# Optimization experiments

Hardware: AMD Instinct MI355X
Metric: run time of the kernel (lower is better)

Reference implementation:

```python
import jax, jax.numpy as jnp
import numpy as np

A2B = 1.8897259886          # angstrom -> bohr
EV2HA = 0.0367493
NUM_RBF = 16
R_MIN = 0.5 * A2B
R_MAX = 4.0 * A2B           # r_max_angstroms=4.0 from gnn_config
RBF_WIDTH = (R_MAX - R_MIN) / NUM_RBF
N_NODES = 100_000
N_EDGES = 3_200_000
EMBED_DIM = 16
N_ELEMS = 4
CODES_PER_ELEM = 4          # all elements are core -> max_codes_per_element
TOTAL_CODES = N_ELEMS * CODES_PER_ELEM
NUM_PAIRS = 10
CODE_OWNER = np.repeat(np.arange(N_ELEMS), CODES_PER_ELEM)  # element owning each code


def setup_inputs() -> dict:
    key = jax.random.key(0)
    ks = jax.random.split(key, 12)
    N, E, D = N_NODES, N_EDGES, EMBED_DIM
    inv_sp = lambda v: np.float32(np.log(np.expm1(v)))  # inverse_softplus
    return {
        "elem_idx": jax.random.randint(ks[0], (N,), 0, N_ELEMS),
        "edge_index": jax.random.randint(ks[1], (2, E), 0, N),
        "distances": jax.random.uniform(ks[2], (E,), minval=1.0, maxval=7.5),  # bohr
        "pair_idx": jax.random.randint(ks[3], (E,), 0, NUM_PAIRS),
        "embed": jax.random.normal(ks[4], (N_ELEMS, D)),
        "fw1": jax.random.normal(ks[5], (D, NUM_RBF)) * 0.3,
        "fb1": jnp.zeros((D,)),
        "fw2": jax.random.normal(ks[6], (D, D)) * 0.3,
        "fb2": jnp.zeros((D,)),
        "mw1": jax.random.normal(ks[7], (D, D)) * 0.3,
        "mb1": jnp.zeros((D,)),
        "mw2": jax.random.normal(ks[8], (3, D)) * 0.05,  # zero-init in orig; small random for a live baseline
        "mb2": jnp.zeros((3,)),
        "codebook": jax.random.normal(ks[9], (TOTAL_CODES, D)),
        "raw_D_e": jnp.full((NUM_PAIRS,), inv_sp(0.1 * EV2HA)),
        "raw_alpha": jnp.full((NUM_PAIRS,), inv_sp(1.5 / A2B)),
        "raw_r0": jnp.full((NUM_PAIRS,), np.float32(3.0 * A2B)),
    }


def reference(elem_idx, edge_index, distances, pair_idx, embed,
              fw1, fb1, fw2, fb2, mw1, mb1, mw2, mb2,
              codebook, raw_D_e, raw_alpha, raw_r0):
    # --- EnvironmentEncoder: gather + edge filter + scatter_add ---
    h = embed[elem_idx]                                              # [N, D]
    centers = jnp.linspace(R_MIN, R_MAX, NUM_RBF, dtype=distances.dtype)
    rbf = jnp.exp(-0.5 * ((distances[:, None] - centers) / RBF_WIDTH) ** 2)  # [E, RBF]
    W = jax.nn.silu(rbf @ fw1.T + fb1) @ fw2.T + fb2                 # [E, D]
    src, tgt = edge_index[0], edge_index[1]
    messages = h[tgt] * W                                            # [E, D]
    agg = jax.ops.segment_sum(messages, src, num_segments=h.shape[0])
    h = h + agg                                                      # [N, D]

    # --- VectorQuantizer (eval path): per-element masked cdist + argmin ---
    d2 = (jnp.sum(h * h, axis=1, keepdims=True)
          - 2.0 * h @ codebook.T
          + jnp.sum(codebook * codebook, axis=1))                    # [N, C] squared dist
    owner = jnp.asarray(CODE_OWNER)
    valid = elem_idx[:, None] == owner[None, :]                      # [N, C]
    atom_types = jnp.argmin(jnp.where(valid, d2, jnp.inf), axis=1)   # [N]
    z_q = codebook[atom_types]                                       # [N, D]
    h_q = h + jax.lax.stop_gradient(z_q - h)                         # straight-through
    # all elements have >1 code -> commitment over all atoms
    vq_loss = 0.25 * jnp.mean((h - jax.lax.stop_gradient(z_q)) ** 2)

    # --- MorseParameterPredictor: edge gather + MLP ---
    pair_feat = h_q[src] + h_q[tgt]                                  # [E, D]
    delta = jax.nn.silu(pair_feat @ mw1.T + mb1) @ mw2.T + mb2       # [E, 3]

    D_e = jax.nn.softplus(raw_D_e[pair_idx] + delta[:, 0])
    alpha = jax.nn.softplus(raw_alpha[pair_idx] + delta[:, 1])
    r0 = raw_r0[pair_idx] + delta[:, 2]
    params = jnp.stack([D_e, alpha, r0], axis=-1)                    # [E, 3]
    return params, vq_loss
```

## Files before the change

kernel.cpp:

```cpp
#include <hip/hip_runtime.h>
#include <stdint.h>

#define A2B   1.8897259886f
#define R_MIN (0.5f * A2B)
#define R_MAX (4.0f * A2B)

#define EPB 2048

__global__ void __launch_bounds__(256) k_bucket(
        const int* __restrict__ src, const int* __restrict__ tgt,
        const int* __restrict__ elem, const float* __restrict__ dist,
        int* __restrict__ gCursor, float* __restrict__ dBuf,
        unsigned short* __restrict__ kBuf, int CAP, int SHIFT, int E)
{
    __shared__ int cnt[256], base_[256];
    int t = threadIdx.x;
    cnt[t] = 0;
    __syncthreads();
    int e0 = blockIdx.x * EPB;
    int eEnd = (e0 + EPB < E) ? e0 + EPB : E;

    float dv[8]; int bv[8]; unsigned short kv[8];
    #pragma unroll
    for (int j = 0; j < 8; ++j) {
        int e = e0 + t + j * 256;
        if (e < eEnd) {
            int s = src[e];
            int q = elem[tgt[e]];
            dv[j] = dist[e];
            int b = s >> SHIFT;
            bv[j] = b;
            kv[j] = (unsigned short)(((s - (b << SHIFT)) << 2) | q);
            atomicAdd(&cnt[b], 1);
        }
    }
    __syncthreads();
    if (cnt[t] > 0) base_[t] = atomicAdd(&gCursor[t], cnt[t]);
    __syncthreads();
    cnt[t] = 0;
    __syncthreads();
    #pragma unroll
    for (int j = 0; j < 8; ++j) {
        int e = e0 + t + j * 256;
        if (e < eEnd) {
            int b = bv[j];
            int pos = base_[b] + atomicAdd(&cnt[b], 1);
            if (pos < CAP) {
                size_t idx = (size_t)b * CAP + pos;
                dBuf[idx] = dv[j];
                kBuf[idx] = kv[j];
            }
        }
    }
}

__global__ void __launch_bounds__(256) k_bscan(
        const int* __restrict__ gCursor, int* __restrict__ bucketBase,
        int* __restrict__ offs, int NBUK, int N, int E)
{
    __shared__ int sd[256];
    int t = threadIdx.x;
    int v = (t < NBUK) ? gCursor[t] : 0;
    sd[t] = v; __syncthreads();
    #pragma unroll
    for (int o = 1; o < 256; o <<= 1) {
        int x = (t >= o) ? sd[t - o] : 0;
        __syncthreads();
        sd[t] += x;
        __syncthreads();
    }
    bucketBase[t] = sd[t] - v;
    if (t == 0) offs[N] = E;
}

__global__ void __launch_bounds__(256) k_bin(
        const float* __restrict__ dBuf, const unsigned short* __restrict__ kBuf,
        const int* __restrict__ gCursor, const int* __restrict__ bucketBase,
        int* __restrict__ offs, float* __restrict__ payload,
        int CAP, int SHIFT, int N)
{
    __shared__ int lcnt[512];
    __shared__ int sd[256];
    int t = threadIdx.x, b = blockIdx.x;
    int n0 = b << SHIFT;
    int n1 = n0 + (1 << SHIFT); if (n1 > N) n1 = N;
    int m  = n1 - n0;
    int cntE = gCursor[b]; if (cntE > CAP) cntE = CAP;
    int base = bucketBase[b];
    for (int i = t; i < m; i += 256) lcnt[i] = 0;
    __syncthreads();
    const float* dB = dBuf + (size_t)b * CAP;
    const unsigned short* kB = kBuf + (size_t)b * CAP;
    for (int i = t; i < cntE; i += 256)
        atomicAdd(&lcnt[kB[i] >> 2], 1);
    __syncthreads();
    int b2 = t * 2;
    int v0 = (b2 < m)     ? lcnt[b2]     : 0;
    int v1 = (b2 + 1 < m) ? lcnt[b2 + 1] : 0;
    int tsum = v0 + v1;
    sd[t] = tsum; __syncthreads();
    #pragma unroll
    for (int o = 1; o < 256; o <<= 1) {
        int x = (t >= o) ? sd[t - o] : 0;
        __syncthreads();
        sd[t] += x;
        __syncthreads();
    }
    int run = sd[t] - tsum;
    if (b2 < m)     { lcnt[b2] = run;     offs[n0 + b2] = base + run;     run += v0; }
    if (b2 + 1 < m) { lcnt[b2 + 1] = run; offs[n0 + b2 + 1] = base + run; run += v1; }
    __syncthreads();
    for (int i = t; i < cntE; i += 256) {
        int kv = kB[i];
        int pos = atomicAdd(&lcnt[kv >> 2], 1);
        unsigned db = __float_as_uint(dB[i]);
        payload[base + pos] = __uint_as_float((db & ~3u) | (unsigned)(kv & 3));
    }
}

__global__ void __launch_bounds__(256) k_gather(
        const int* __restrict__ elem, const float* __restrict__ embed,
        const float* __restrict__ codebook,
        const float* __restrict__ fw1, const float* __restrict__ fb1,
        const float* __restrict__ fw2, const float* __restrict__ fb2,
        const int* __restrict__ offs, const float* __restrict__ payload,
        int* __restrict__ atype, float* __restrict__ loss, int N)
{
    __shared__ float4 s_fw1t[64];
    __shared__ float4 s_fw2v[64];
    __shared__ float s_cb[256];
    __shared__ float s_fb1[16], s_fb2[16], s_emb[64], s_cbn[16];
    __shared__ float s_red[4];
    int t = threadIdx.x;
    {
        float* f1 = (float*)s_fw1t;
        f1[(t & 15) * 16 + (t >> 4)] = fw1[t];
        float* f2 = (float*)s_fw2v;
        f2[t] = fw2[t];
        s_cb[t] = codebook[t];
    }
    if (t < 16) { s_fb1[t] = fb1[t]; s_fb2[t] = fb2[t]; }
    if (t < 64) s_emb[t] = embed[t];
    __syncthreads();
    if (t < 16) {
        float s = 0.f;
        #pragma unroll
        for (int j = 0; j < 16; ++j) { float c = s_cb[t * 16 + j]; s += c * c; }
        s_cbn[t] = s;
    }
    __syncthreads();

    int node = blockIdx.x * 64 + (t >> 2);
    int sub  = t & 3;
    float lp = 0.0f;
    if (node < N) {
        int o0 = offs[node], o1 = offs[node + 1];
        float G0[16], G1[16], G2[16], G3[16];
        #pragma unroll
        for (int j = 0; j < 16; ++j) { G0[j]=0.f; G1[j]=0.f; G2[j]=0.f; G3[j]=0.f; }
        float c0 = 0.f, c1 = 0.f, c2 = 0.f, c3 = 0.f;

        const float invw   = 16.0f / (R_MAX - R_MIN);
        const float u0base = R_MIN * invw;
        const float kstep  = 16.0f / 15.0f;
        for (int i = o0 + sub; i < o1; i += 8) {
            int ii = i + 4;
            bool has2 = (ii < o1);
            unsigned p0 = __float_as_uint(payload[i]);
            unsigned p1 = has2 ? __float_as_uint(payload[ii]) : p0;
            int q0 = (int)(p0 & 3u), q1 = (int)(p1 & 3u);
            float d0 = __uint_as_float(p0 & ~3u);
            float d1 = __uint_as_float(p1 & ~3u);
            float ua = d0 * invw - u0base;
            float ub = d1 * invw - u0base;
            float g0[16], g1[16];
            #pragma unroll
            for (int i2 = 0; i2 < 16; ++i2) { g0[i2] = s_fb1[i2]; g1[i2] = s_fb1[i2]; }
            #pragma clang loop unroll(disable)
            for (int k = 0; k < 16; ++k) {
                float r0 = __expf(-0.5f * ua * ua);
                float r1 = __expf(-0.5f * ub * ub);
                float4 w0 = s_fw1t[k*4+0], w1 = s_fw1t[k*4+1];
                float4 w2 = s_fw1t[k*4+2], w3 = s_fw1t[k*4+3];
                g0[0]+=r0*w0.x;  g0[1]+=r0*w0.y;  g0[2]+=r0*w0.z;  g0[3]+=r0*w0.w;
                g0[4]+=r0*w1.x;  g0[5]+=r0*w1.y;  g0[6]+=r0*w1.z;  g0[7]+=r0*w1.w;
                g0[8]+=r0*w2.x;  g0[9]+=r0*w2.y;  g0[10]+=r0*w2.z; g0[11]+=r0*w2.w;
                g0[12]+=r0*w3.x; g0[13]+=r0*w3.y; g0[14]+=r0*w3.z; g0[15]+=r0*w3.w;
                g1[0]+=r1*w0.x;  g1[1]+=r1*w0.y;  g1[2]+=r1*w0.z;  g1[3]+=r1*w0.w;
                g1[4]+=r1*w1.x;  g1[5]+=r1*w1.y;  g1[6]+=r1*w1.z;  g1[7]+=r1*w1.w;
                g1[8]+=r1*w2.x;  g1[9]+=r1*w2.y;  g1[10]+=r1*w2.z; g1[11]+=r1*w2.w;
                g1[12]+=r1*w3.x; g1[13]+=r1*w3.y; g1[14]+=r1*w3.z; g1[15]+=r1*w3.w;
                ua -= kstep; ub -= kstep;
            }
            {
                float m0 = (q0==0)?1.f:0.f, m1 = (q0==1)?1.f:0.f;
                float m2 = (q0==2)?1.f:0.f, m3 = (q0==3)?1.f:0.f;
                c0 += m0; c1 += m1; c2 += m2; c3 += m3;
                #pragma unroll
                for (int i2 = 0; i2 < 16; ++i2) {
                    float a = g0[i2];
                    float s = a * __builtin_amdgcn_rcpf(1.0f + __expf(-a));
                    G0[i2] += m0*s; G1[i2] += m1*s; G2[i2] += m2*s; G3[i2] += m3*s;
                }
            }
            if (has2) {
                float m0 = (q1==0)?1.f:0.f, m1 = (q1==1)?1.f:0.f;
                float m2 = (q1==2)?1.f:0.f, m3 = (q1==3)?1.f:0.f;
                c0 += m0; c1 += m1; c2 += m2; c3 += m3;
                #pragma unroll
                for (int i2 = 0; i2 < 16; ++i2) {
                    float a = g1[i2];
                    float s = a * __builtin_amdgcn_rcpf(1.0f + __expf(-a));
                    G0[i2] += m0*s; G1[i2] += m1*s; G2[i2] += m2*s; G3[i2] += m3*s;
                }
            }
        }
        #pragma unroll
        for (int mm = 1; mm <= 2; mm <<= 1) {
            #pragma unroll
            for (int j = 0; j < 16; ++j) {
                G0[j] += __shfl_xor(G0[j], mm, 64);
                G1[j] += __shfl_xor(G1[j], mm, 64);
                G2[j] += __shfl_xor(G2[j], mm, 64);
                G3[j] += __shfl_xor(G3[j], mm, 64);
            }
            c0 += __shfl_xor(c0, mm, 64);
            c1 += __shfl_xor(c1, mm, 64);
            c2 += __shfl_xor(c2, mm, 64);
            c3 += __shfl_xor(c3, mm, 64);
        }
        float Gs[16];
        #pragma unroll
        for (int j = 0; j < 16; ++j)
            Gs[j] = (sub==0) ? G0[j] : (sub==1) ? G1[j] : (sub==2) ? G2[j] : G3[j];
        float cs = (sub==0) ? c0 : (sub==1) ? c1 : (sub==2) ? c2 : c3;
        const float* er = s_emb + sub * 16;
        float acc[16];
        #pragma clang loop unroll_count(4)
        for (int j = 0; j < 16; ++j) {
            float4 f0 = s_fw2v[j*4+0], f1 = s_fw2v[j*4+1];
            float4 f2 = s_fw2v[j*4+2], f3 = s_fw2v[j*4+3];
            float w = Gs[0]*f0.x  + Gs[1]*f0.y  + Gs[2]*f0.z  + Gs[3]*f0.w
                    + Gs[4]*f1.x  + Gs[5]*f1.y  + Gs[6]*f1.z  + Gs[7]*f1.w
                    + Gs[8]*f2.x  + Gs[9]*f2.y  + Gs[10]*f2.z + Gs[11]*f2.w
                    + Gs[12]*f3.x + Gs[13]*f3.y + Gs[14]*f3.z + Gs[15]*f3.w;
            acc[j] = (w + cs * s_fb2[j]) * er[j];
        }
        #pragma unroll
        for (int mm = 1; mm <= 2; mm <<= 1) {
            #pragma unroll
            for (int j = 0; j < 16; ++j)
                acc[j] += __shfl_xor(acc[j], mm, 64);
        }
        int qn = elem[node];
        float h[16], hh = 0.f;
        #pragma unroll
        for (int j = 0; j < 16; ++j) {
            h[j] = acc[j] + s_emb[qn * 16 + j];
            hh += h[j] * h[j];
        }
        float best = __builtin_inff(); int bi = 0;
        #pragma unroll
        for (int c = 0; c < 4; ++c) {
            int code = qn * 4 + c;
            float dot = 0.f;
            #pragma unroll
            for (int j = 0; j < 16; ++j) dot += h[j] * s_cb[code * 16 + j];
            float d2 = hh - 2.0f * dot + s_cbn[code];
            if (d2 < best) { best = d2; bi = code; }
        }
        if (sub == 0) {
            atype[node] = bi;
            #pragma unroll
            for (int j = 0; j < 16; ++j) {
                float df = h[j] - s_cb[bi * 16 + j];
                lp += df * df;
            }
        }
    }
    #pragma unroll
    for (int o = 32; o > 0; o >>= 1) lp += __shfl_down(lp, o, 64);
    int wid = t >> 6;
    if ((t & 63) == 0) s_red[wid] = lp;
    __syncthreads();
    if (t == 0) atomicAdd(loss, s_red[0] + s_red[1] + s_red[2] + s_red[3]);
}

__global__ void __launch_bounds__(256) k_table(
        const float* __restrict__ codebook,
        const float* __restrict__ mw1, const float* __restrict__ mb1,
        const float* __restrict__ mw2, const float* __restrict__ mb2,
        const float* __restrict__ rD, const float* __restrict__ rA,
        const float* __restrict__ rR,
        const float* __restrict__ loss, float4* __restrict__ table,
        float* __restrict__ out_loss, float inv_nd)
{
    __shared__ float s_cb[256], s_mw1[256], s_mb1[16], s_mw2[48], s_mb2[3];
    __shared__ float s_rd[10], s_ra[10], s_rr[10];
    int tid = threadIdx.x;
    s_cb[tid] = codebook[tid];
    s_mw1[tid] = mw1[tid];
    if (tid < 16) s_mb1[tid] = mb1[tid];
    if (tid < 48) s_mw2[tid] = mw2[tid];
    if (tid < 3)  s_mb2[tid] = mb2[tid];
    if (tid < 10) { s_rd[tid] = rD[tid]; s_ra[tid] = rA[tid]; s_rr[tid] = rR[tid]; }
    __syncthreads();

    int a = tid >> 4, b = tid & 15;
    float pf[16];
    #pragma unroll
    for (int j = 0; j < 16; ++j) pf[j] = s_cb[a * 16 + j] + s_cb[b * 16 + j];
    float hid[16];
    #pragma unroll
    for (int i = 0; i < 16; ++i) {
        float acc = s_mb1[i];
        #pragma unroll
        for (int j = 0; j < 16; ++j) acc += pf[j] * s_mw1[i * 16 + j];
        hid[i] = acc / (1.0f + __expf(-acc));
    }
    float del[3];
    #pragma unroll
    for (int r = 0; r < 3; ++r) {
        float acc = s_mb2[r];
        #pragma unroll
        for (int i = 0; i < 16; ++i) acc += hid[i] * s_mw2[r * 16 + i];
        del[r] = acc;
    }
    #pragma unroll
    for (int p = 0; p < 10; ++p) {
        float xd = s_rd[p] + del[0];
        float xa = s_ra[p] + del[1];
        float De = (xd > 20.f) ? xd : log1pf(__expf(xd));
        float al = (xa > 20.f) ? xa : log1pf(__expf(xa));
        float r0 = s_rr[p] + del[2];
        table[tid * 10 + p] = make_float4(De, al, r0, 0.f);
    }
    if (tid == 0) out_loss[0] = 0.25f * loss[0] * inv_nd;
}

__global__ void __launch_bounds__(256) k_out(
        const int* __restrict__ src, const int* __restrict__ tgt,
        const int* __restrict__ pidx, const int* __restrict__ atype,
        const float4* __restrict__ table, float2* __restrict__ out, int Ehalf)
{
    int i = blockIdx.x * 256 + threadIdx.x;
    if (i >= Ehalf) return;
    int2 s2 = ((const int2*)src)[i];
    int2 t2 = ((const int2*)tgt)[i];
    int2 p2 = ((const int2*)pidx)[i];
    int i0 = (atype[s2.x] * 16 + atype[t2.x]) * 10 + p2.x;
    int i1 = (atype[s2.y] * 16 + atype[t2.y]) * 10 + p2.y;
    float4 t0 = table[i0];
    float4 t1 = table[i1];
    float2* op = out + (size_t)3 * i;
    op[0] = make_float2(t0.x, t0.y);
    op[1] = make_float2(t0.z, t1.x);
    op[2] = make_float2(t1.y, t1.z);
}

extern "C" void kernel_launch(void* const* d_in, const int* in_sizes, int n_in,
                              void* d_out, int out_size, void* d_ws, size_t ws_size,
                              hipStream_t stream)
{
    (void)n_in;
    const int*   elem  = (const int*)d_in[0];
    const int*   eidx  = (const int*)d_in[1];
    const float* dist  = (const float*)d_in[2];
    const int*   pidx  = (const int*)d_in[3];
    const float* embed = (const float*)d_in[4];
    const float* fw1   = (const float*)d_in[5];
    const float* fb1   = (const float*)d_in[6];
    const float* fw2   = (const float*)d_in[7];
    const float* fb2   = (const float*)d_in[8];
    const float* mw1   = (const float*)d_in[9];
    const float* mb1   = (const float*)d_in[10];
    const float* mw2   = (const float*)d_in[11];
    const float* mb2   = (const float*)d_in[12];
    const float* cb    = (const float*)d_in[13];
    const float* rD    = (const float*)d_in[14];
    const float* rA    = (const float*)d_in[15];
    const float* rR    = (const float*)d_in[16];

    int N = in_sizes[0];
    int E = in_sizes[2];
    const int* src = eidx;
    const int* tgt = eidx + E;

    int SHIFT = 0;
    while ((1 << SHIFT) < (N + 255) / 256) SHIFT++;
    int NBUK = (N + (1 << SHIFT) - 1) >> SHIFT;
    long long expv = ((long long)E << SHIFT) / N;
    int CAP = (int)(expv + expv / 16 + 256);

    size_t outBytes = (size_t)out_size * 4;
    char* ob = (char*)d_out;
    size_t oc = 0;
    float* dBuf = (float*)(ob + oc);           oc += (size_t)NBUK * CAP * 4;
    unsigned short* kBuf = (unsigned short*)(ob + oc); oc += (size_t)NBUK * CAP * 2;
    oc = (oc + 3) & ~(size_t)3;
    float* payload = (float*)(ob + oc);        oc += (size_t)E * 4;
    int*   offs    = (int*)(ob + oc);          oc += (size_t)(N + 1) * 4;
    if (oc > outBytes) return;

    char* ws = (char*)d_ws;
    size_t cur = 0;
    int*   gCursor    = (int*)(ws + cur);  cur += 256 * 4;
    float* loss       = (float*)(ws + cur); cur += 4;
    size_t clearB = cur;
    int*   bucketBase = (int*)(ws + cur);  cur += 256 * 4;
    int*   atype      = (int*)(ws + cur);  cur += (size_t)N * 4;
    cur = (cur + 15) & ~(size_t)15;
    float4* table     = (float4*)(ws + cur); cur += 2560 * sizeof(float4);
    if (ws_size < cur) return;

    hipMemsetAsync(d_ws, 0, clearB, stream);

    k_bucket<<<(E + EPB - 1) / EPB, 256, 0, stream>>>(
        src, tgt, elem, dist, gCursor, dBuf, kBuf, CAP, SHIFT, E);
    k_bscan<<<1, 256, 0, stream>>>(gCursor, bucketBase, offs, NBUK, N, E);
    k_bin<<<NBUK, 256, 0, stream>>>(dBuf, kBuf, gCursor, bucketBase,
                                    offs, payload, CAP, SHIFT, N);
    k_gather<<<(N + 63) / 64, 256, 0, stream>>>(elem, embed, cb, fw1, fb1,
                                                fw2, fb2, offs, payload,
                                                atype, loss, N);
    float* outl = (float*)d_out + (size_t)3 * E;
    k_table<<<1, 256, 0, stream>>>(cb, mw1, mb1, mw2, mb2, rD, rA, rR,
                                   loss, table, outl,
                                   1.0f / (float)((size_t)N * 16));
    k_out<<<(E / 2 + 255) / 256, 256, 0, stream>>>(src, tgt, pidx, atype, table,
                                                   (float2*)d_out, E / 2);
}
```

Baseline: 259.7 us.

## Privatize per-wave bucket counters and degree-sort nodes within gather blocks

The bucketing kernel now keeps a separate shared counter array for each wavefront, which cuts LDS atomic contention, and derives per-wave base offsets from a single global atomic per bucket. The gather kernel bitonic-sorts its 64 nodes by degree in shared memory and assigns them to wavefronts in that order, so nodes with similar edge counts share a wave and lanes sit idle less often. The cost is extra shared memory and about 21 barrier-separated sort steps per block.

```diff
diff --git a/kernel.cpp b/kernel.cpp
--- a/kernel.cpp
+++ b/kernel.cpp
@@ -13,9 +13,10 @@
         int* __restrict__ gCursor, float* __restrict__ dBuf,
         unsigned short* __restrict__ kBuf, int CAP, int SHIFT, int E)
 {
-    __shared__ int cnt[256], base_[256];
+    __shared__ int cnt[4][256], sbase[4][256];
     int t = threadIdx.x;
-    cnt[t] = 0;
+    int w = t >> 6;
+    cnt[0][t] = 0; cnt[1][t] = 0; cnt[2][t] = 0; cnt[3][t] = 0;
     __syncthreads();
     int e0 = blockIdx.x * EPB;
     int eEnd = (e0 + EPB < E) ? e0 + EPB : E;
@@ -31,20 +32,27 @@
             int b = s >> SHIFT;
             bv[j] = b;
             kv[j] = (unsigned short)(((s - (b << SHIFT)) << 2) | q);
-            atomicAdd(&cnt[b], 1);
-        }
-    }
-    __syncthreads();
-    if (cnt[t] > 0) base_[t] = atomicAdd(&gCursor[t], cnt[t]);
-    __syncthreads();
-    cnt[t] = 0;
+            atomicAdd(&cnt[w][b], 1);
+        }
+    }
+    __syncthreads();
+    {
+        int c0 = cnt[0][t], c1 = cnt[1][t], c2 = cnt[2][t], c3 = cnt[3][t];
+        int tot = c0 + c1 + c2 + c3;
+        int g = (tot > 0) ? atomicAdd(&gCursor[t], tot) : 0;
+        sbase[0][t] = g;
+        sbase[1][t] = g + c0;
+        sbase[2][t] = g + c0 + c1;
+        sbase[3][t] = g + c0 + c1 + c2;
+        cnt[0][t] = 0; cnt[1][t] = 0; cnt[2][t] = 0; cnt[3][t] = 0;
+    }
     __syncthreads();
     #pragma unroll
     for (int j = 0; j < 8; ++j) {
         int e = e0 + t + j * 256;
         if (e < eEnd) {
             int b = bv[j];
-            int pos = base_[b] + atomicAdd(&cnt[b], 1);
+            int pos = sbase[w][b] + atomicAdd(&cnt[w][b], 1);
             if (pos < CAP) {
                 size_t idx = (size_t)b * CAP + pos;
                 dBuf[idx] = dv[j];
@@ -131,6 +139,7 @@
     __shared__ float s_cb[256];
     __shared__ float s_fb1[16], s_fb2[16], s_emb[64], s_cbn[16];
     __shared__ float s_red[4];
+    __shared__ int s_ord[64];
     int t = threadIdx.x;
     {
         float* f1 = (float*)s_fw1t;
@@ -141,6 +150,12 @@
     }
     if (t < 16) { s_fb1[t] = fb1[t]; s_fb2[t] = fb2[t]; }
     if (t < 64) s_emb[t] = embed[t];
+    int nbase = blockIdx.x * 64;
+    if (t < 64) {
+        int n = nbase + t;
+        int dg = (n < N) ? (offs[n + 1] - offs[n]) : 0x7FFF;
+        s_ord[t] = (dg << 6) | t;
+    }
     __syncthreads();
     if (t < 16) {
         float s = 0.f;
@@ -148,9 +163,22 @@
         for (int j = 0; j < 16; ++j) { float c = s_cb[t * 16 + j]; s += c * c; }
         s_cbn[t] = s;
     }
-    __syncthreads();
-
-    int node = blockIdx.x * 64 + (t >> 2);
+    for (int ksz = 2; ksz <= 64; ksz <<= 1) {
+        for (int jj = ksz >> 1; jj > 0; jj >>= 1) {
+            __syncthreads();
+            if (t < 64) {
+                int ixj = t ^ jj;
+                if (ixj > t) {
+                    int a = s_ord[t], b = s_ord[ixj];
+                    bool asc = ((t & ksz) == 0);
+                    if (asc ? (a > b) : (a < b)) { s_ord[t] = b; s_ord[ixj] = a; }
+                }
+            }
+        }
+    }
+    __syncthreads();
+
+    int node = nbase + (s_ord[t >> 2] & 63);
     int sub  = t & 3;
     float lp = 0.0f;
     if (node < N) {
```

Measured after the change: 255.5 us. No clear change (-1.6%).

## Fuse binning into gather with 128-node buckets sorted in shared memory

Applied to the files above, without the earlier changes.

Replaces the three-pass bucket/scan/bin pipeline with a single coarse bucketing pass into 128-node buckets, then has each gather block do the local histogram, prefix scan and scatter of payloads into shared memory before computing. Nodes within a block are bitonic-sorted by degree so the four lanes per node see balanced work. This removes two kernel launches and the global payload/offs round trip. In exchange, k_bucket reads src twice, the fw1 filter weights are read from global memory instead of LDS, the per-bucket capacity is clamped to the shared buffer size so overflow edges would be dropped, and the large shared buffer may limit occupancy.

```diff
diff --git a/kernel.cpp b/kernel.cpp
--- a/kernel.cpp
+++ b/kernel.cpp
@@ -5,142 +5,71 @@
 #define R_MIN (0.5f * A2B)
 #define R_MAX (4.0f * A2B)
 
-#define EPB 2048
+#define EPB   16384
+#define BSH   7
+#define BN    128
 
 __global__ void __launch_bounds__(256) k_bucket(
         const int* __restrict__ src, const int* __restrict__ tgt,
         const int* __restrict__ elem, const float* __restrict__ dist,
+        const float* __restrict__ fw1, float* __restrict__ fw1t,
         int* __restrict__ gCursor, float* __restrict__ dBuf,
-        unsigned short* __restrict__ kBuf, int CAP, int SHIFT, int E)
+        unsigned char* __restrict__ lBuf, int CAP, int NBUK, int E)
 {
-    __shared__ int cnt[256], base_[256];
+    __shared__ int cnt[1024], sbase[1024];
     int t = threadIdx.x;
-    cnt[t] = 0;
+    if (blockIdx.x == 0)
+        fw1t[t] = fw1[(t & 15) * 16 + (t >> 4)];
+    for (int i = t; i < NBUK; i += 256) cnt[i] = 0;
     __syncthreads();
     int e0 = blockIdx.x * EPB;
     int eEnd = (e0 + EPB < E) ? e0 + EPB : E;
-
-    float dv[8]; int bv[8]; unsigned short kv[8];
-    #pragma unroll
-    for (int j = 0; j < 8; ++j) {
-        int e = e0 + t + j * 256;
-        if (e < eEnd) {
-            int s = src[e];
-            int q = elem[tgt[e]];
-            dv[j] = dist[e];
-            int b = s >> SHIFT;
-            bv[j] = b;
-            kv[j] = (unsigned short)(((s - (b << SHIFT)) << 2) | q);
-            atomicAdd(&cnt[b], 1);
-        }
-    }
-    __syncthreads();
-    if (cnt[t] > 0) base_[t] = atomicAdd(&gCursor[t], cnt[t]);
-    __syncthreads();
-    cnt[t] = 0;
-    __syncthreads();
-    #pragma unroll
-    for (int j = 0; j < 8; ++j) {
-        int e = e0 + t + j * 256;
-        if (e < eEnd) {
-            int b = bv[j];
-            int pos = base_[b] + atomicAdd(&cnt[b], 1);
-            if (pos < CAP) {
-                size_t idx = (size_t)b * CAP + pos;
-                dBuf[idx] = dv[j];
-                kBuf[idx] = kv[j];
-            }
+    for (int e = e0 + t; e < eEnd; e += 256)
+        atomicAdd(&cnt[src[e] >> BSH], 1);
+    __syncthreads();
+    for (int i = t; i < NBUK; i += 256) {
+        int c = cnt[i];
+        sbase[i] = c ? atomicAdd(&gCursor[i], c) : 0;
+        cnt[i] = 0;
+    }
+    __syncthreads();
+    for (int e = e0 + t; e < eEnd; e += 256) {
+        int s = src[e];
+        int b = s >> BSH;
+        int q = elem[tgt[e]];
+        float d = dist[e];
+        int pos = sbase[b] + atomicAdd(&cnt[b], 1);
+        if (pos < CAP) {
+            size_t idx = (size_t)b * CAP + pos;
+            dBuf[idx] = __uint_as_float((__float_as_uint(d) & ~3u) | (unsigned)q);
+            lBuf[idx] = (unsigned char)(s & (BN - 1));
         }
     }
 }
 
-__global__ void __launch_bounds__(256) k_bscan(
-        const int* __restrict__ gCursor, int* __restrict__ bucketBase,
-        int* __restrict__ offs, int NBUK, int N, int E)
-{
-    __shared__ int sd[256];
-    int t = threadIdx.x;
-    int v = (t < NBUK) ? gCursor[t] : 0;
-    sd[t] = v; __syncthreads();
-    #pragma unroll
-    for (int o = 1; o < 256; o <<= 1) {
-        int x = (t >= o) ? sd[t - o] : 0;
-        __syncthreads();
-        sd[t] += x;
-        __syncthreads();
-    }
-    bucketBase[t] = sd[t] - v;
-    if (t == 0) offs[N] = E;
-}
-
-__global__ void __launch_bounds__(256) k_bin(
-        const float* __restrict__ dBuf, const unsigned short* __restrict__ kBuf,
-        const int* __restrict__ gCursor, const int* __restrict__ bucketBase,
-        int* __restrict__ offs, float* __restrict__ payload,
-        int CAP, int SHIFT, int N)
-{
-    __shared__ int lcnt[512];
-    __shared__ int sd[256];
-    int t = threadIdx.x, b = blockIdx.x;
-    int n0 = b << SHIFT;
-    int n1 = n0 + (1 << SHIFT); if (n1 > N) n1 = N;
-    int m  = n1 - n0;
-    int cntE = gCursor[b]; if (cntE > CAP) cntE = CAP;
-    int base = bucketBase[b];
-    for (int i = t; i < m; i += 256) lcnt[i] = 0;
-    __syncthreads();
-    const float* dB = dBuf + (size_t)b * CAP;
-    const unsigned short* kB = kBuf + (size_t)b * CAP;
-    for (int i = t; i < cntE; i += 256)
-        atomicAdd(&lcnt[kB[i] >> 2], 1);
-    __syncthreads();
-    int b2 = t * 2;
-    int v0 = (b2 < m)     ? lcnt[b2]     : 0;
-    int v1 = (b2 + 1 < m) ? lcnt[b2 + 1] : 0;
-    int tsum = v0 + v1;
-    sd[t] = tsum; __syncthreads();
-    #pragma unroll
-    for (int o = 1; o < 256; o <<= 1) {
-        int x = (t >= o) ? sd[t - o] : 0;
-        __syncthreads();
-        sd[t] += x;
-        __syncthreads();
-    }
-    int run = sd[t] - tsum;
-    if (b2 < m)     { lcnt[b2] = run;     offs[n0 + b2] = base + run;     run += v0; }
-    if (b2 + 1 < m) { lcnt[b2 + 1] = run; offs[n0 + b2 + 1] = base + run; run += v1; }
-    __syncthreads();
-    for (int i = t; i < cntE; i += 256) {
-        int kv = kB[i];
-        int pos = atomicAdd(&lcnt[kv >> 2], 1);
-        unsigned db = __float_as_uint(dB[i]);
-        payload[base + pos] = __uint_as_float((db & ~3u) | (unsigned)(kv & 3));
-    }
-}
-
-__global__ void __launch_bounds__(256) k_gather(
+__global__ void __launch_bounds__(512) k_gather(
         const int* __restrict__ elem, const float* __restrict__ embed,
         const float* __restrict__ codebook,
-        const float* __restrict__ fw1, const float* __restrict__ fb1,
+        const float4* __restrict__ fw1t4, const float* __restrict__ fb1,
         const float* __restrict__ fw2, const float* __restrict__ fb2,
-        const int* __restrict__ offs, const float* __restrict__ payload,
-        int* __restrict__ atype, float* __restrict__ loss, int N)
+        const int* __restrict__ gCursor, const float* __restrict__ dBuf,
+        const unsigned char* __restrict__ lBuf,
+        int* __restrict__ atype, float* __restrict__ loss, int CAP, int N)
 {
-    __shared__ float4 s_fw1t[64];
+    __shared__ float s_pay[4864];
     __shared__ float4 s_fw2v[64];
     __shared__ float s_cb[256];
     __shared__ float s_fb1[16], s_fb2[16], s_emb[64], s_cbn[16];
-    __shared__ float s_red[4];
+    __shared__ float s_red[8];
+    __shared__ int lhist[BN], loff[BN + 1], sd2[BN], s_ord[BN];
     int t = threadIdx.x;
-    {
-        float* f1 = (float*)s_fw1t;
-        f1[(t & 15) * 16 + (t >> 4)] = fw1[t];
-        float* f2 = (float*)s_fw2v;
-        f2[t] = fw2[t];
+    if (t < 256) {
+        ((float*)s_fw2v)[t] = fw2[t];
         s_cb[t] = codebook[t];
     }
     if (t < 16) { s_fb1[t] = fb1[t]; s_fb2[t] = fb2[t]; }
     if (t < 64) s_emb[t] = embed[t];
+    if (t < BN) lhist[t] = 0;
     __syncthreads();
     if (t < 16) {
         float s = 0.f;
@@ -148,13 +77,58 @@
         for (int j = 0; j < 16; ++j) { float c = s_cb[t * 16 + j]; s += c * c; }
         s_cbn[t] = s;
     }
-    __syncthreads();
-
-    int node = blockIdx.x * 64 + (t >> 2);
+
+    int b = blockIdx.x;
+    int n0 = b << BSH;
+    int cntE = gCursor[b]; if (cntE > CAP) cntE = CAP;
+    size_t base = (size_t)b * CAP;
+
+    for (int i = t; i < cntE; i += 512)
+        atomicAdd(&lhist[lBuf[base + i]], 1);
+    __syncthreads();
+    int vdeg = 0;
+    if (t < BN) {
+        vdeg = lhist[t];
+        sd2[t] = vdeg;
+        s_ord[t] = (vdeg << 8) | t;
+    }
+    __syncthreads();
+    #pragma unroll
+    for (int o = 1; o < BN; o <<= 1) {
+        int x = (t < BN && t >= o) ? sd2[t - o] : 0;
+        __syncthreads();
+        if (t < BN) sd2[t] += x;
+        __syncthreads();
+    }
+    if (t < BN) { int ex = sd2[t] - vdeg; loff[t] = ex; lhist[t] = ex; }
+    if (t == 0) loff[BN] = cntE;
+    __syncthreads();
+    for (int i = t; i < cntE; i += 512) {
+        int l = lBuf[base + i];
+        int pos = atomicAdd(&lhist[l], 1);
+        s_pay[pos] = dBuf[base + i];
+    }
+    for (int ksz = 2; ksz <= BN; ksz <<= 1) {
+        for (int jj = ksz >> 1; jj > 0; jj >>= 1) {
+            __syncthreads();
+            if (t < BN) {
+                int ixj = t ^ jj;
+                if (ixj > t) {
+                    int a = s_ord[t], c = s_ord[ixj];
+                    bool asc = ((t & ksz) == 0);
+                    if (asc ? (a > c) : (a < c)) { s_ord[t] = c; s_ord[ixj] = a; }
+                }
+            }
+        }
+    }
+    __syncthreads();
+
+    int l = s_ord[t >> 2] & 255;
+    int node = n0 + l;
     int sub  = t & 3;
     float lp = 0.0f;
     if (node < N) {
-        int o0 = offs[node], o1 = offs[node + 1];
+        int o0 = loff[l], o1 = loff[l + 1];
         float G0[16], G1[16], G2[16], G3[16];
         #pragma unroll
         for (int j = 0; j < 16; ++j) { G0[j]=0.f; G1[j]=0.f; G2[j]=0.f; G3[j]=0.f; }
@@ -166,8 +140,8 @@
         for (int i = o0 + sub; i < o1; i += 8) {
             int ii = i + 4;
             bool has2 = (ii < o1);
-            unsigned p0 = __float_as_uint(payload[i]);
-            unsigned p1 = has2 ? __float_as_uint(payload[ii]) : p0;
+            unsigned p0 = __float_as_uint(s_pay[i]);
+            unsigned p1 = has2 ? __float_as_uint(s_pay[ii]) : p0;
             int q0 = (int)(p0 & 3u), q1 = (int)(p1 & 3u);
             float d0 = __uint_as_float(p0 & ~3u);
             float d1 = __uint_as_float(p1 & ~3u);
@@ -180,8 +154,8 @@
             for (int k = 0; k < 16; ++k) {
                 float r0 = __expf(-0.5f * ua * ua);
                 float r1 = __expf(-0.5f * ub * ub);
-                float4 w0 = s_fw1t[k*4+0], w1 = s_fw1t[k*4+1];
-                float4 w2 = s_fw1t[k*4+2], w3 = s_fw1t[k*4+3];
+                float4 w0 = fw1t4[k*4+0], w1 = fw1t4[k*4+1];
+                float4 w2 = fw1t4[k*4+2], w3 = fw1t4[k*4+3];
                 g0[0]+=r0*w0.x;  g0[1]+=r0*w0.y;  g0[2]+=r0*w0.z;  g0[3]+=r0*w0.w;
                 g0[4]+=r0*w1.x;  g0[5]+=r0*w1.y;  g0[6]+=r0*w1.z;  g0[7]+=r0*w1.w;
                 g0[8]+=r0*w2.x;  g0[9]+=r0*w2.y;  g0[10]+=r0*w2.z; g0[11]+=r0*w2.w;
@@ -283,7 +257,12 @@
     int wid = t >> 6;
     if ((t & 63) == 0) s_red[wid] = lp;
     __syncthreads();
-    if (t == 0) atomicAdd(loss, s_red[0] + s_red[1] + s_red[2] + s_red[3]);
+    if (t == 0) {
+        float s = 0.f;
+        #pragma unroll
+        for (int wq = 0; wq < 8; ++wq) s += s_red[wq];
+        atomicAdd(loss, s);
+    }
 }
 
 __global__ void __launch_bounds__(256) k_table(
@@ -386,43 +365,39 @@
     const int* src = eidx;
     const int* tgt = eidx + E;
 
-    int SHIFT = 0;
-    while ((1 << SHIFT) < (N + 255) / 256) SHIFT++;
-    int NBUK = (N + (1 << SHIFT) - 1) >> SHIFT;
-    long long expv = ((long long)E << SHIFT) / N;
-    int CAP = (int)(expv + expv / 16 + 256);
+    int NBUK = (N + BN - 1) >> BSH;
+    if (NBUK > 1024) return;
+    long long expv = ((long long)E << BSH) / N;
+    int CAP = (int)(expv + expv / 8 + 256);
+    if (CAP > 4864) CAP = 4864;
 
     size_t outBytes = (size_t)out_size * 4;
     char* ob = (char*)d_out;
     size_t oc = 0;
-    float* dBuf = (float*)(ob + oc);           oc += (size_t)NBUK * CAP * 4;
-    unsigned short* kBuf = (unsigned short*)(ob + oc); oc += (size_t)NBUK * CAP * 2;
-    oc = (oc + 3) & ~(size_t)3;
-    float* payload = (float*)(ob + oc);        oc += (size_t)E * 4;
-    int*   offs    = (int*)(ob + oc);          oc += (size_t)(N + 1) * 4;
+    float* dBuf = (float*)(ob + oc);               oc += (size_t)NBUK * CAP * 4;
+    unsigned char* lBuf = (unsigned char*)(ob + oc); oc += (size_t)NBUK * CAP;
     if (oc > outBytes) return;
 
     char* ws = (char*)d_ws;
     size_t cur = 0;
-    int*   gCursor    = (int*)(ws + cur);  cur += 256 * 4;
-    float* loss       = (float*)(ws + cur); cur += 4;
+    int*   gCursor = (int*)(ws + cur);  cur += 1024 * 4;
+    float* loss    = (float*)(ws + cur); cur += 4;
     size_t clearB = cur;
-    int*   bucketBase = (int*)(ws + cur);  cur += 256 * 4;
-    int*   atype      = (int*)(ws + cur);  cur += (size_t)N * 4;
     cur = (cur + 15) & ~(size_t)15;
-    float4* table     = (float4*)(ws + cur); cur += 2560 * sizeof(float4);
+    float* fw1t    = (float*)(ws + cur); cur += 256 * 4;
+    int*   atype   = (int*)(ws + cur);  cur += (size_t)N * 4;
+    cur = (cur + 15) & ~(size_t)15;
+    float4* table  = (float4*)(ws + cur); cur += 2560 * sizeof(float4);
     if (ws_size < cur) return;
 
     hipMemsetAsync(d_ws, 0, clearB, stream);
 
     k_bucket<<<(E + EPB - 1) / EPB, 256, 0, stream>>>(
-        src, tgt, elem, dist, gCursor, dBuf, kBuf, CAP, SHIFT, E);
-    k_bscan<<<1, 256, 0, stream>>>(gCursor, bucketBase, offs, NBUK, N, E);
-    k_bin<<<NBUK, 256, 0, stream>>>(dBuf, kBuf, gCursor, bucketBase,
-                                    offs, payload, CAP, SHIFT, N);
-    k_gather<<<(N + 63) / 64, 256, 0, stream>>>(elem, embed, cb, fw1, fb1,
-                                                fw2, fb2, offs, payload,
-                                                atype, loss, N);
+        src, tgt, elem, dist, fw1, fw1t, gCursor, dBuf, lBuf, CAP, NBUK, E);
+    k_gather<<<NBUK, 512, 0, stream>>>(elem, embed, cb,
+                                       (const float4*)fw1t, fb1, fw2, fb2,
+                                       gCursor, dBuf, lBuf, atype, loss,
+                                       CAP, N);
     float* outl = (float*)d_out + (size_t)3 * E;
     k_table<<<1, 256, 0, stream>>>(cb, mw1, mb1, mw2, mb2, rD, rA, rR,
                                    loss, table, outl,
```

Result: slower. 288.8 us (+11.2%).
